# Kernel optimization log

Hardware: AMD Instinct MI355X
Metric: run time of the kernel (lower is better)

The kernel has to match this reference:

```python
import jax, jax.numpy as jnp
import numpy as np

DIM = 128; HEADS = 8; WS = 8; SHIFT = 4; B = 8; H = 256; W = 256; T = 1


def _rel_index(ws):
    # faithful port of create_relative_position_index
    coords = np.arange(ws)
    yy, xx = np.meshgrid(coords, coords, indexing='ij')
    cf = np.stack([yy.reshape(-1), xx.reshape(-1)])          # (2, ws*ws)
    rel = cf[:, :, None] - cf[:, None, :]                     # (2, N, N)
    rel[0] += ws - 1
    rel[1] += ws - 1
    return rel[0] * (2 * ws - 1) + rel[1]                     # (N, N) int


def _row_mask(ws, shift):
    jj, ii = np.meshgrid(np.arange(ws), np.arange(ws), indexing='ij')
    return ((jj >= ws - shift) | (ii >= ws - shift)).reshape(-1)  # (N,) bool


def layernorm(x, g, b, eps=1e-5):
    mu = x.mean(-1, keepdims=True)
    var = ((x - mu) ** 2).mean(-1, keepdims=True)
    return (x - mu) * jax.lax.rsqrt(var + eps) * g + b


def setup_inputs() -> dict:
    key = jax.random.key(0)
    ks = jax.random.split(key, 16)
    s = 0.02
    d = DIM
    inp = {
        'x': jax.random.normal(ks[0], (B, T, H, W, d), jnp.float32),
        'wq': jax.random.normal(ks[1], (d, d), jnp.float32) * s,
        'bq': jnp.zeros((d,), jnp.float32),
        'wk': jax.random.normal(ks[2], (d, d), jnp.float32) * s,
        'bk': jnp.zeros((d,), jnp.float32),
        'wv': jax.random.normal(ks[3], (d, d), jnp.float32) * s,
        'bv': jnp.zeros((d,), jnp.float32),
        'wp': jax.random.normal(ks[4], (d, d), jnp.float32) * s,
        'bp': jnp.zeros((d,), jnp.float32),
        'rpb': jax.random.normal(ks[5], (2 * WS - 1, 2 * WS - 1, HEADS), jnp.float32) * s,
        'ln1_g': jnp.ones((d,), jnp.float32),
        'ln1_b': jnp.zeros((d,), jnp.float32),
        'ln2_g': jnp.ones((d,), jnp.float32),
        'ln2_b': jnp.zeros((d,), jnp.float32),
        'w1': jax.random.normal(ks[6], (d, 4 * d), jnp.float32) * s,
        'b1': jnp.zeros((4 * d,), jnp.float32),
        'w2': jax.random.normal(ks[7], (4 * d, d), jnp.float32) * s,
        'b2': jnp.zeros((d,), jnp.float32),
        'gate': jax.random.normal(ks[8], (1, H, W, 1), jnp.float32) * s,
    }
    return inp


def reference(x, wq, bq, wk, bk, wv, bv, wp, bp, rpb, ln1_g, ln1_b, ln2_g, ln2_b, w1, b1, w2, b2, gate):
    Bx, Tx, Hx, Wx, C = x.shape
    skip = x[:, 0]                                             # (B,H,W,C)
    xn = layernorm(x, ln1_g, ln1_b)[:, 0]                      # (B,H,W,C)
    xs = jnp.roll(xn, (-SHIFT, -SHIFT), axis=(1, 2))
    nh, nw, N = Hx // WS, Wx // WS, WS * WS
    # window partition -> (B*nh*nw, N, C)
    xw = xs.reshape(Bx, nh, WS, nw, WS, C).transpose(0, 1, 3, 2, 4, 5).reshape(-1, N, C)
    hd = C // HEADS
    scale = hd ** -0.5
    q = (xw @ wq + bq).reshape(-1, N, HEADS, hd)
    k = (xw @ wk + bk).reshape(-1, N, HEADS, hd)
    v = (xw @ wv + bv).reshape(-1, N, HEADS, hd)
    attn = jnp.einsum('bnhc,bmhc->bnhm', q, k) * scale         # (Bw,N,H,N)
    # relative position bias gather; .view(B,N,heads,N) over (N*N,heads) flat layout
    idx = jnp.asarray(_rel_index(WS).reshape(-1))
    bias = rpb.reshape(-1, HEADS)[idx].reshape(N, HEADS, N)
    attn = attn + bias[None]
    # shift mask: full query rows set to -1e9 (per original patch_mask)
    rmask = jnp.asarray(_row_mask(WS, SHIFT))
    attn = jnp.where(rmask[None, :, None, None], jnp.float32(-1e9), attn)
    attn = jax.nn.softmax(attn, axis=-1)
    out = jnp.einsum('bnhm,bmhc->bnhc', attn, v).reshape(-1, N, C) @ wp + bp
    # window reverse
    xr = out.reshape(Bx, nh, nw, WS, WS, C).transpose(0, 1, 3, 2, 4, 5).reshape(Bx, Hx, Wx, C)
    xa = xs + xr
    xa = jnp.roll(xa, (SHIFT, SHIFT), axis=(1, 2))
    # gated skip
    x2 = xa + jax.nn.sigmoid(gate) * skip
    # MLP (dropout = identity in eval)
    h = jax.nn.gelu(layernorm(x2, ln2_g, ln2_b) @ w1 + b1, approximate=False)
    y = x2 + (h @ w2 + b2)
    return y.reshape(Bx, Tx, Hx, Wx, C)
```

## Files before the change

### kernel.cpp

```cpp
#include <hip/hip_runtime.h>
#include <hip/hip_bf16.h>
#include <math.h>

#define TPB 256

typedef __attribute__((ext_vector_type(8))) __bf16 bf16x8;
typedef __attribute__((ext_vector_type(4))) float f32x4;

static __device__ __forceinline__ bf16x8 lds_frag(const char* base, int row, int byteOff, int rowBytes) {
    return *reinterpret_cast<const bf16x8*>(base + row * rowBytes + (byteOff ^ ((row & 7) << 4)));
}
static __device__ __forceinline__ void lds_wr_bf16(char* base, int row, int col, int rowBytes, float v) {
    *reinterpret_cast<__bf16*>(base + row * rowBytes + ((col << 1) ^ ((row & 7) << 4))) = (__bf16)v;
}

__global__ void convert_w(const float* __restrict__ wq, const float* __restrict__ wk,
                          const float* __restrict__ wv, const float* __restrict__ wp,
                          const float* __restrict__ w1, const float* __restrict__ w2,
                          const float* __restrict__ rpb, const float* __restrict__ bq,
                          __bf16* __restrict__ ws)
{
    int g = blockIdx.x * 256 + threadIdx.x;
    if (g < 65536) {
        int which = g >> 14, idx = g & 16383, n = idx >> 7, k = idx & 127;
        const float* W = (which == 0) ? wq : (which == 1) ? wk : (which == 2) ? wv : wp;
        float v = W[k * 128 + n];
        if (which == 0) v *= 0.25f;
        ws[g] = (__bf16)v;
    } else if (g < 131072) {
        int idx = g - 65536, n = idx >> 7, k = idx & 127;
        ws[g] = (__bf16)w1[k * 512 + n];
    } else if (g < 196608) {
        int idx = g - 131072, n = idx >> 9, k = idx & 511;
        ws[g] = (__bf16)w2[k * 128 + n];
    } else if (g < 204800) {
        float* wsf = (float*)(ws + 196608);
        int g2 = g - 196608;
        int hc = g2 >> 8, h = hc >> 2, ct = hc & 3;
        int lane = (g2 >> 2) & 63, kg = lane >> 4, ar = lane & 15, r = g2 & 3;
        int dy = kg - h + 7;
        int dx = r - (ct * 2 + (ar >> 3)) + 7;
        wsf[g2] = rpb[(dy * 15 + dx) * 8 + (ar & 7)];
    } else if (g < 204928) {
        float* wsf = (float*)(ws + 196608);
        wsf[8192 + (g - 204800)] = bq[g - 204800] * 0.25f;
    }
}

#define O_K     0
#define O_VT    16384
#define O_XN    32768
#define O_H     16384
#define O_ATTN  49152
#define O_PROJ  57344
#define O_Q     66320
#define O_P     70416
#define O_MU    78608
#define O_RS    78864
#define O_GATE  79120
#define O_BASE  79376
#define SMEM_SZ 79632

__global__ __launch_bounds__(TPB, 2) void swin_fused_kernel(
    const float* __restrict__ x,
    const __bf16* __restrict__ wqT,
    const __bf16* __restrict__ wkT, const float* __restrict__ bk,
    const __bf16* __restrict__ wvT, const float* __restrict__ bv,
    const __bf16* __restrict__ wpT, const float* __restrict__ bp,
    const float* __restrict__ bias_pre, const float* __restrict__ bqs,
    const float* __restrict__ ln1g, const float* __restrict__ ln1b,
    const float* __restrict__ ln2g, const float* __restrict__ ln2b,
    const __bf16* __restrict__ w1T, const float* __restrict__ b1,
    const __bf16* __restrict__ w2T, const float* __restrict__ b2,
    const float* __restrict__ gate,
    float* __restrict__ out)
{
    __shared__ __align__(16) char smem[SMEM_SZ];
    char* s_k    = smem + O_K;
    char* s_vT   = smem + O_VT;
    char* s_xn   = smem + O_XN;
    char* s_h    = smem + O_H;
    char* s_attn = smem + O_ATTN;
    float* s_proj = (float*)(smem + O_PROJ);
    char* s_q    = smem + O_Q;
    float* s_out  = (float*)(smem);
    float* s_mu   = (float*)(smem + O_MU);
    float* s_rs   = (float*)(smem + O_RS);
    float* s_gate = (float*)(smem + O_GATE);
    int*   s_base = (int*)(smem + O_BASE);

    const int tid = threadIdx.x;
    const int blk = blockIdx.x;
    const int b  = blk >> 10;
    const int wh = (blk >> 5) & 31;
    const int ww = blk & 31;

    const int row = tid >> 2;
    const int l4  = tid & 3;
    float vals[32];

    {
        const int si = wh * 8 + (row >> 3), sj = ww * 8 + (row & 7);
        const int oi = (si + 4) & 255, oj = (sj + 4) & 255;
        const int base = ((b * 256 + oi) * 256 + oj) * 128;
        if (l4 == 0) { s_base[row] = base; s_gate[row] = gate[oi * 256 + oj]; }
        const float* xp = x + base + l4 * 32;
        float sum = 0.f, sq = 0.f;
#pragma unroll
        for (int i = 0; i < 8; ++i) {
            const float4 v4 = reinterpret_cast<const float4*>(xp)[i];
            vals[4*i+0] = v4.x; vals[4*i+1] = v4.y; vals[4*i+2] = v4.z; vals[4*i+3] = v4.w;
            sum += v4.x + v4.y + v4.z + v4.w;
            sq  += v4.x*v4.x + v4.y*v4.y + v4.z*v4.z + v4.w*v4.w;
        }
        sum += __shfl_xor(sum, 1); sum += __shfl_xor(sum, 2);
        sq  += __shfl_xor(sq , 1); sq  += __shfl_xor(sq , 2);
        const float mu  = sum * (1.f / 128.f);
        const float var = sq * (1.f / 128.f) - mu * mu;
        const float rs  = rsqrtf(var + 1e-5f);
        if (l4 == 0) { s_mu[row] = mu; s_rs[row] = rs; }
#pragma unroll
        for (int j = 0; j < 4; ++j) {
            bf16x8 pk;
#pragma unroll
            for (int e = 0; e < 8; ++e) {
                const int d = l4 * 32 + j * 8 + e;
                pk[e] = (__bf16)((vals[j*8+e] - mu) * rs * ln1g[d] + ln1b[d]);
            }
            const int byteOff = (l4 * 64 + j * 16) ^ ((row & 7) << 4);
            *reinterpret_cast<bf16x8*>(s_xn + row * 256 + byteOff) = pk;
        }
    }
    __syncthreads();

    const int lane = tid & 63, w = tid >> 6;
    const int ar = lane & 15, kg = lane >> 4;

    float vm[2];

    {
        bf16x8 a[4][4];
#pragma unroll
        for (int rt = 0; rt < 4; ++rt)
#pragma unroll
            for (int kc = 0; kc < 4; ++kc)
                a[rt][kc] = lds_frag(s_xn, rt * 16 + ar, kc * 64 + (kg << 4), 256);
        const int nrow = ((ar >> 2) << 3) + (ar & 3);
        bf16x8 aq[4];
#pragma unroll
        for (int kc = 0; kc < 4; ++kc)
            aq[kc] = lds_frag(s_xn, nrow, kc * 64 + (kg << 4), 256);

#pragma unroll
        for (int ct2 = 0; ct2 < 2; ++ct2) {
            const int brow = (w + ct2 * 4) * 16 + ar;
            bf16x8 bf[4];
#pragma unroll
            for (int kc = 0; kc < 4; ++kc)
                bf[kc] = *reinterpret_cast<const bf16x8*>(wkT + brow * 128 + kc * 32 + (kg << 3));
            const float bb = bk[brow];
#pragma unroll
            for (int rt = 0; rt < 4; ++rt) {
                f32x4 c = {bb, bb, bb, bb};
#pragma unroll
                for (int kc = 0; kc < 4; ++kc)
                    c = __builtin_amdgcn_mfma_f32_16x16x32_bf16(a[rt][kc], bf[kc], c, 0, 0, 0);
#pragma unroll
                for (int r = 0; r < 4; ++r)
                    lds_wr_bf16(s_k, rt*16 + kg*4 + r, brow, 256, c[r]);
            }
        }
#pragma unroll
        for (int ct2 = 0; ct2 < 2; ++ct2) {
            const int brow = (w + ct2 * 4) * 16 + ar;
            bf16x8 bf[4];
#pragma unroll
            for (int kc = 0; kc < 4; ++kc)
                bf[kc] = *reinterpret_cast<const bf16x8*>(wvT + brow * 128 + kc * 32 + (kg << 3));
            const float bb = bv[brow];
            float vs = 0.f;
#pragma unroll
            for (int rt = 0; rt < 4; ++rt) {
                f32x4 c = {bb, bb, bb, bb};
#pragma unroll
                for (int kc = 0; kc < 4; ++kc)
                    c = __builtin_amdgcn_mfma_f32_16x16x32_bf16(a[rt][kc], bf[kc], c, 0, 0, 0);
#pragma unroll
                for (int r = 0; r < 4; ++r) {
                    lds_wr_bf16(s_vT, brow, rt*16 + kg*4 + r, 128, c[r]);
                    vs += c[r];
                }
            }
            vs += __shfl_xor(vs, 16); vs += __shfl_xor(vs, 32);
            vm[ct2] = vs * (1.f / 64.f);
        }
#pragma unroll
        for (int ct2 = 0; ct2 < 2; ++ct2) {
            const int brow = (w + ct2 * 4) * 16 + ar;
            bf16x8 bf[4];
#pragma unroll
            for (int kc = 0; kc < 4; ++kc)
                bf[kc] = *reinterpret_cast<const bf16x8*>(wqT + brow * 128 + kc * 32 + (kg << 3));
            const float bb = bqs[brow];
            f32x4 c = {bb, bb, bb, bb};
#pragma unroll
            for (int kc = 0; kc < 4; ++kc)
                c = __builtin_amdgcn_mfma_f32_16x16x32_bf16(aq[kc], bf[kc], c, 0, 0, 0);
#pragma unroll
            for (int r = 0; r < 4; ++r)
                lds_wr_bf16(s_q, kg*4 + r, brow, 256, c[r]);
        }
    }
    __syncthreads();

    if (kg == 0) {
#pragma unroll
        for (int ct2 = 0; ct2 < 2; ++ct2)
            lds_wr_bf16(s_attn, 16, (w + ct2 * 4) * 16 + ar, 256, vm[ct2]);
    }

    char* s_p = smem + O_P + (w << 11);
#pragma unroll
    for (int hi = 0; hi < 2; ++hi) {
        const int h = w + hi * 4;
        bf16x8 aQ = {};
        if (lane < 32) aQ = lds_frag(s_q, ar, h * 32 + (kg << 4), 256);
        f32x4 sc[4];
#pragma unroll
        for (int ct = 0; ct < 4; ++ct) {
            bf16x8 bK = {};
            if (lane < 32) bK = lds_frag(s_k, ct * 16 + ar, h * 32 + (kg << 4), 256);
            const f32x4 cin = *reinterpret_cast<const f32x4*>(bias_pre + ((h * 4 + ct) << 8) + (lane << 2));
            sc[ct] = __builtin_amdgcn_mfma_f32_16x16x32_bf16(aQ, bK, cin, 0, 0, 0);
        }
        float s[4] = {0.f, 0.f, 0.f, 0.f};
#pragma unroll
        for (int ct = 0; ct < 4; ++ct)
#pragma unroll
            for (int r = 0; r < 4; ++r) {
                sc[ct][r] = __expf(sc[ct][r]);
                s[r] += sc[ct][r];
            }
#pragma unroll
        for (int r = 0; r < 4; ++r) {
            s[r] += __shfl_xor(s[r], 1); s[r] += __shfl_xor(s[r], 2);
            s[r] += __shfl_xor(s[r], 4); s[r] += __shfl_xor(s[r], 8);
            const float inv = 1.f / s[r];
#pragma unroll
            for (int ct = 0; ct < 4; ++ct)
                lds_wr_bf16(s_p, kg*4 + r, ct*16 + ar, 128, sc[ct][r] * inv);
        }
        f32x4 o = {0.f, 0.f, 0.f, 0.f};
#pragma unroll
        for (int kc = 0; kc < 2; ++kc) {
            bf16x8 ap = lds_frag(s_p, ar, kc * 64 + (kg << 4), 128);
            bf16x8 bV = lds_frag(s_vT, h * 16 + ar, kc * 64 + (kg << 4), 128);
            o = __builtin_amdgcn_mfma_f32_16x16x32_bf16(ap, bV, o, 0, 0, 0);
        }
#pragma unroll
        for (int r = 0; r < 4; ++r)
            lds_wr_bf16(s_attn, kg*4 + r, h*16 + ar, 256, o[r]);
    }
    __syncthreads();

    {
        bf16x8 a2[2][4];
#pragma unroll
        for (int rt = 0; rt < 2; ++rt)
#pragma unroll
            for (int kc = 0; kc < 4; ++kc)
                a2[rt][kc] = lds_frag(s_attn, rt * 16 + ar, kc * 64 + (kg << 4), 256);
#pragma unroll
        for (int ct2 = 0; ct2 < 2; ++ct2) {
            const int brow = (w + ct2 * 4) * 16 + ar;
            bf16x8 bf[4];
#pragma unroll
            for (int kc = 0; kc < 4; ++kc)
                bf[kc] = *reinterpret_cast<const bf16x8*>(wpT + brow * 128 + kc * 32 + (kg << 3));
            const float bb = bp[brow];
#pragma unroll
            for (int rt = 0; rt < 2; ++rt) {
                f32x4 c = {bb, bb, bb, bb};
#pragma unroll
                for (int kc = 0; kc < 4; ++kc)
                    c = __builtin_amdgcn_mfma_f32_16x16x32_bf16(a2[rt][kc], bf[kc], c, 0, 0, 0);
                if (rt == 0) {
#pragma unroll
                    for (int r = 0; r < 4; ++r)
                        s_proj[(kg*4 + r) * 132 + brow] = c[r];
                } else if (kg == 0) {
                    s_proj[16 * 132 + brow] = c[0];
                }
            }
        }
    }
    __syncthreads();

    {
        const float sg = 1.f / (1.f + __expf(-s_gate[row]));
        const float mu1 = s_mu[row], rs1 = s_rs[row];
        const bool masked = ((row >> 3) >= 4) || ((row & 7) >= 4);
        const int prow = masked ? 16 : ((row >> 3) * 4 + (row & 7));
        const float* pr = s_proj + prow * 132 + l4 * 32;
        const float* g1  = ln1g + l4 * 32;
        const float* b1v = ln1b + l4 * 32;
        float sum = 0.f, sq = 0.f;
#pragma unroll
        for (int i = 0; i < 8; ++i) {
            const float4 gg = reinterpret_cast<const float4*>(g1)[i];
            const float4 bb = reinterpret_cast<const float4*>(b1v)[i];
            const float g4[4] = {gg.x, gg.y, gg.z, gg.w};
            const float b4[4] = {bb.x, bb.y, bb.z, bb.w};
#pragma unroll
            for (int c = 0; c < 4; ++c) {
                const int idx = 4*i + c;
                const float xv = vals[idx];
                const float xnv = (xv - mu1) * rs1 * g4[c] + b4[c];
                const float x2 = xnv + pr[idx] + sg * xv;
                vals[idx] = x2;
                sum += x2; sq += x2 * x2;
            }
        }
        sum += __shfl_xor(sum, 1); sum += __shfl_xor(sum, 2);
        sq  += __shfl_xor(sq , 1); sq  += __shfl_xor(sq , 2);
        const float mu  = sum * (1.f / 128.f);
        const float var = sq * (1.f / 128.f) - mu * mu;
        const float rs  = rsqrtf(var + 1e-5f);
#pragma unroll
        for (int j = 0; j < 4; ++j) {
            bf16x8 pk;
#pragma unroll
            for (int e = 0; e < 8; ++e) {
                const int d = l4 * 32 + j * 8 + e;
                pk[e] = (__bf16)((vals[j*8+e] - mu) * rs * ln2g[d] + ln2b[d]);
            }
            const int byteOff = (l4 * 64 + j * 16) ^ ((row & 7) << 4);
            *reinterpret_cast<bf16x8*>(s_k + row * 256 + byteOff) = pk;
        }
    }
    __syncthreads();

    bf16x8 a[4][4];
#pragma unroll
    for (int rt = 0; rt < 4; ++rt)
#pragma unroll
        for (int kc = 0; kc < 4; ++kc)
            a[rt][kc] = lds_frag(s_k, rt * 16 + ar, kc * 64 + (kg << 4), 256);

    f32x4 acc2[2][4];
#pragma unroll
    for (int ct2 = 0; ct2 < 2; ++ct2) {
        const float bb = b2[(w + ct2 * 4) * 16 + ar];
#pragma unroll
        for (int rt = 0; rt < 4; ++rt) acc2[ct2][rt] = {bb, bb, bb, bb};
    }

#pragma unroll
    for (int hh = 0; hh < 2; ++hh) {
#pragma unroll
        for (int i = 0; i < 4; ++i) {
            const int ct = hh * 16 + w + 4 * i;
            const int brow = ct * 16 + ar;
            bf16x8 bfr[4];
#pragma unroll
            for (int kc = 0; kc < 4; ++kc)
                bfr[kc] = *reinterpret_cast<const bf16x8*>(w1T + brow * 128 + kc * 32 + (kg << 3));
            const float bb = b1[brow];
#pragma unroll
            for (int rt = 0; rt < 4; ++rt) {
                f32x4 c = {bb, bb, bb, bb};
#pragma unroll
                for (int kc = 0; kc < 4; ++kc)
                    c = __builtin_amdgcn_mfma_f32_16x16x32_bf16(a[rt][kc], bfr[kc], c, 0, 0, 0);
#pragma unroll
                for (int r = 0; r < 4; ++r) {
                    const float v = c[r];
                    const float t = 0.7978845608028654f * (v + 0.044715f * v * v * v);
                    const float th = 1.f - 2.f / (__expf(2.f * t) + 1.f);
                    lds_wr_bf16(s_h, rt * 16 + kg * 4 + r, brow - hh * 256, 512, 0.5f * v * (1.f + th));
                }
            }
        }
        __syncthreads();
#pragma unroll
        for (int kc = 0; kc < 8; ++kc) {
            bf16x8 ah[4];
#pragma unroll
            for (int rt = 0; rt < 4; ++rt)
                ah[rt] = lds_frag(s_h, rt * 16 + ar, kc * 64 + (kg << 4), 512);
#pragma unroll
            for (int ct2 = 0; ct2 < 2; ++ct2) {
                const int brow = (w + ct2 * 4) * 16 + ar;
                const bf16x8 bw = *reinterpret_cast<const bf16x8*>(w2T + brow * 512 + hh * 256 + kc * 32 + (kg << 3));
#pragma unroll
                for (int rt = 0; rt < 4; ++rt)
                    acc2[ct2][rt] = __builtin_amdgcn_mfma_f32_16x16x32_bf16(ah[rt], bw, acc2[ct2][rt], 0, 0, 0);
            }
        }
        __syncthreads();
    }

#pragma unroll
    for (int ct2 = 0; ct2 < 2; ++ct2)
#pragma unroll
        for (int rt = 0; rt < 4; ++rt)
#pragma unroll
            for (int r = 0; r < 4; ++r)
                s_out[(rt * 16 + kg * 4 + r) * 132 + (w + ct2 * 4) * 16 + ar] = acc2[ct2][rt][r];
    __syncthreads();
    {
        const int base = s_base[row];
        float* op = out + base + l4 * 32;
        const float* po = s_out + row * 132 + l4 * 32;
#pragma unroll
        for (int i = 0; i < 8; ++i) {
            float4 o;
            o.x = vals[4*i+0] + po[4*i+0];
            o.y = vals[4*i+1] + po[4*i+1];
            o.z = vals[4*i+2] + po[4*i+2];
            o.w = vals[4*i+3] + po[4*i+3];
            reinterpret_cast<float4*>(op)[i] = o;
        }
    }
}

extern "C" void kernel_launch(void* const* d_in, const int* in_sizes, int n_in,
                              void* d_out, int out_size, void* d_ws, size_t ws_size,
                              hipStream_t stream) {
    (void)in_sizes; (void)n_in; (void)ws_size; (void)out_size;
    const float* x    = (const float*)d_in[0];
    const float* wq   = (const float*)d_in[1];
    const float* bq   = (const float*)d_in[2];
    const float* wk   = (const float*)d_in[3];
    const float* bk   = (const float*)d_in[4];
    const float* wv   = (const float*)d_in[5];
    const float* bv   = (const float*)d_in[6];
    const float* wp   = (const float*)d_in[7];
    const float* bp   = (const float*)d_in[8];
    const float* rpb  = (const float*)d_in[9];
    const float* ln1g = (const float*)d_in[10];
    const float* ln1b = (const float*)d_in[11];
    const float* ln2g = (const float*)d_in[12];
    const float* ln2b = (const float*)d_in[13];
    const float* w1   = (const float*)d_in[14];
    const float* b1   = (const float*)d_in[15];
    const float* w2   = (const float*)d_in[16];
    const float* b2   = (const float*)d_in[17];
    const float* gate = (const float*)d_in[18];
    float* out = (float*)d_out;

    __bf16* ws = (__bf16*)d_ws;
    const __bf16* wqT = ws;
    const __bf16* wkT = ws + 16384;
    const __bf16* wvT = ws + 32768;
    const __bf16* wpT = ws + 49152;
    const __bf16* w1T = ws + 65536;
    const __bf16* w2T = ws + 131072;
    const float* wsf  = (const float*)(ws + 196608);
    const float* bias_pre = wsf;
    const float* bqs      = wsf + 8192;

    convert_w<<<801, 256, 0, stream>>>(wq, wk, wv, wp, w1, w2, rpb, bq, ws);
    swin_fused_kernel<<<8192, TPB, 0, stream>>>(x, wqT, wkT, bk, wvT, bv, wpT, bp,
                                                bias_pre, bqs, ln1g, ln1b, ln2g, ln2b,
                                                w1T, b1, w2T, b2, gate, out);
}
```

Before: 701.1 us.

## Swap MFMA operands for packed LDS writes and shrink shared memory for 3 blocks/CU

Several GEMMs now pass the weight tile as the A operand and the activation as B. Each lane then holds four consecutive output columns and can write them to LDS as one packed bf16x4 store instead of four scalar bf16 stores. The shared-memory layout is overlapped more tightly, cutting it from about 79.6KB to about 50.7KB, and launch bounds are raised to 3 blocks per CU. The masked-row output is now computed as the V-mean times Wp in a scalar loop, and the relative-bias precompute layout is permuted to match. The changes add an extra __syncthreads and register pressure under the tighter occupancy bound, which risks spills.

```diff
diff --git a/kernel.cpp b/kernel.cpp
--- a/kernel.cpp
+++ b/kernel.cpp
@@ -5,13 +5,16 @@
 #define TPB 256
 
 typedef __attribute__((ext_vector_type(8))) __bf16 bf16x8;
+typedef __attribute__((ext_vector_type(4))) __bf16 bf16x4;
 typedef __attribute__((ext_vector_type(4))) float f32x4;
 
 static __device__ __forceinline__ bf16x8 lds_frag(const char* base, int row, int byteOff, int rowBytes) {
     return *reinterpret_cast<const bf16x8*>(base + row * rowBytes + (byteOff ^ ((row & 7) << 4)));
 }
-static __device__ __forceinline__ void lds_wr_bf16(char* base, int row, int col, int rowBytes, float v) {
-    *reinterpret_cast<__bf16*>(base + row * rowBytes + ((col << 1) ^ ((row & 7) << 4))) = (__bf16)v;
+static __device__ __forceinline__ void lds_wr4(char* base, int row, int col0, int rowBytes, f32x4 v) {
+    bf16x4 p;
+    p[0] = (__bf16)v[0]; p[1] = (__bf16)v[1]; p[2] = (__bf16)v[2]; p[3] = (__bf16)v[3];
+    *reinterpret_cast<bf16x4*>(base + row * rowBytes + ((col0 << 1) ^ ((row & 7) << 4))) = p;
 }
 
 __global__ void convert_w(const float* __restrict__ wq, const float* __restrict__ wk,
@@ -38,30 +41,26 @@
         int g2 = g - 196608;
         int hc = g2 >> 8, h = hc >> 2, ct = hc & 3;
         int lane = (g2 >> 2) & 63, kg = lane >> 4, ar = lane & 15, r = g2 & 3;
-        int dy = kg - h + 7;
-        int dx = r - (ct * 2 + (ar >> 3)) + 7;
-        wsf[g2] = rpb[(dy * 15 + dx) * 8 + (ar & 7)];
+        int dy = (ar >> 2) - h + 7;
+        int dx = (ar & 3) - (ct * 2 + (kg >> 1)) + 7;
+        int hsrc = ((kg & 1) << 2) | r;
+        wsf[g2] = rpb[(dy * 15 + dx) * 8 + hsrc];
     } else if (g < 204928) {
         float* wsf = (float*)(ws + 196608);
         wsf[8192 + (g - 204800)] = bq[g - 204800] * 0.25f;
     }
 }
 
-#define O_K     0
-#define O_VT    16384
-#define O_XN    32768
-#define O_H     16384
-#define O_ATTN  49152
-#define O_PROJ  57344
-#define O_Q     66320
-#define O_P     70416
-#define O_MU    78608
-#define O_RS    78864
-#define O_GATE  79120
-#define O_BASE  79376
-#define SMEM_SZ 79632
-
-__global__ __launch_bounds__(TPB, 2) void swin_fused_kernel(
+#define O_P     4096
+#define O_ATTN  12288
+#define O_MU    49152
+#define O_RS    49408
+#define O_GATE  49664
+#define O_BASE  49920
+#define O_VMEAN 50176
+#define SMEM_SZ 50688
+
+__global__ __launch_bounds__(TPB, 3) void swin_fused_kernel(
     const float* __restrict__ x,
     const __bf16* __restrict__ wqT,
     const __bf16* __restrict__ wkT, const float* __restrict__ bk,
@@ -76,18 +75,20 @@
     float* __restrict__ out)
 {
     __shared__ __align__(16) char smem[SMEM_SZ];
-    char* s_k    = smem + O_K;
-    char* s_vT   = smem + O_VT;
-    char* s_xn   = smem + O_XN;
-    char* s_h    = smem + O_H;
+    char* s_xn   = smem;
+    char* s_q    = smem;
+    char* s_k    = smem + 16384;
+    char* s_vT   = smem + 32768;
+    char* s_xn2  = smem + 32768;
     char* s_attn = smem + O_ATTN;
-    float* s_proj = (float*)(smem + O_PROJ);
-    char* s_q    = smem + O_Q;
+    char* s_h    = smem;
+    float* s_proj = (float*)(smem);
     float* s_out  = (float*)(smem);
     float* s_mu   = (float*)(smem + O_MU);
     float* s_rs   = (float*)(smem + O_RS);
     float* s_gate = (float*)(smem + O_GATE);
     int*   s_base = (int*)(smem + O_BASE);
+    float* s_vmean = (float*)(smem + O_VMEAN);
 
     const int tid = threadIdx.x;
     const int blk = blockIdx.x;
@@ -136,46 +137,42 @@
     const int lane = tid & 63, w = tid >> 6;
     const int ar = lane & 15, kg = lane >> 4;
 
-    float vm[2];
-
-    {
-        bf16x8 a[4][4];
-#pragma unroll
-        for (int rt = 0; rt < 4; ++rt)
-#pragma unroll
-            for (int kc = 0; kc < 4; ++kc)
-                a[rt][kc] = lds_frag(s_xn, rt * 16 + ar, kc * 64 + (kg << 4), 256);
+    bf16x8 a[4][4];
+    bf16x8 aq[4];
+    {
+#pragma unroll
+        for (int nt = 0; nt < 4; ++nt)
+#pragma unroll
+            for (int kc = 0; kc < 4; ++kc)
+                a[nt][kc] = lds_frag(s_xn, nt * 16 + ar, kc * 64 + (kg << 4), 256);
         const int nrow = ((ar >> 2) << 3) + (ar & 3);
-        bf16x8 aq[4];
 #pragma unroll
         for (int kc = 0; kc < 4; ++kc)
             aq[kc] = lds_frag(s_xn, nrow, kc * 64 + (kg << 4), 256);
 
+#pragma unroll
+        for (int ct2 = 0; ct2 < 2; ++ct2) {
+            const int m0t = (w + ct2 * 4) * 16;
+            bf16x8 af[4];
+#pragma unroll
+            for (int kc = 0; kc < 4; ++kc)
+                af[kc] = *reinterpret_cast<const bf16x8*>(wkT + (m0t + ar) * 128 + kc * 32 + (kg << 3));
+            const float4 bb4 = *reinterpret_cast<const float4*>(bk + m0t + kg * 4);
+#pragma unroll
+            for (int nt = 0; nt < 4; ++nt) {
+                f32x4 c = {bb4.x, bb4.y, bb4.z, bb4.w};
+#pragma unroll
+                for (int kc = 0; kc < 4; ++kc)
+                    c = __builtin_amdgcn_mfma_f32_16x16x32_bf16(af[kc], a[nt][kc], c, 0, 0, 0);
+                lds_wr4(s_k, nt * 16 + ar, m0t + kg * 4, 256, c);
+            }
+        }
 #pragma unroll
         for (int ct2 = 0; ct2 < 2; ++ct2) {
             const int brow = (w + ct2 * 4) * 16 + ar;
             bf16x8 bf[4];
 #pragma unroll
             for (int kc = 0; kc < 4; ++kc)
-                bf[kc] = *reinterpret_cast<const bf16x8*>(wkT + brow * 128 + kc * 32 + (kg << 3));
-            const float bb = bk[brow];
-#pragma unroll
-            for (int rt = 0; rt < 4; ++rt) {
-                f32x4 c = {bb, bb, bb, bb};
-#pragma unroll
-                for (int kc = 0; kc < 4; ++kc)
-                    c = __builtin_amdgcn_mfma_f32_16x16x32_bf16(a[rt][kc], bf[kc], c, 0, 0, 0);
-#pragma unroll
-                for (int r = 0; r < 4; ++r)
-                    lds_wr_bf16(s_k, rt*16 + kg*4 + r, brow, 256, c[r]);
-            }
-        }
-#pragma unroll
-        for (int ct2 = 0; ct2 < 2; ++ct2) {
-            const int brow = (w + ct2 * 4) * 16 + ar;
-            bf16x8 bf[4];
-#pragma unroll
-            for (int kc = 0; kc < 4; ++kc)
                 bf[kc] = *reinterpret_cast<const bf16x8*>(wvT + brow * 128 + kc * 32 + (kg << 3));
             const float bb = bv[brow];
             float vs = 0.f;
@@ -185,39 +182,32 @@
 #pragma unroll
                 for (int kc = 0; kc < 4; ++kc)
                     c = __builtin_amdgcn_mfma_f32_16x16x32_bf16(a[rt][kc], bf[kc], c, 0, 0, 0);
-#pragma unroll
-                for (int r = 0; r < 4; ++r) {
-                    lds_wr_bf16(s_vT, brow, rt*16 + kg*4 + r, 128, c[r]);
-                    vs += c[r];
-                }
+                lds_wr4(s_vT, brow, rt * 16 + kg * 4, 128, c);
+                vs += c[0] + c[1] + c[2] + c[3];
             }
             vs += __shfl_xor(vs, 16); vs += __shfl_xor(vs, 32);
-            vm[ct2] = vs * (1.f / 64.f);
-        }
+            if (kg == 0) s_vmean[brow] = vs * (1.f / 64.f);
+        }
+    }
+    __syncthreads();
+
+    {
 #pragma unroll
         for (int ct2 = 0; ct2 < 2; ++ct2) {
-            const int brow = (w + ct2 * 4) * 16 + ar;
-            bf16x8 bf[4];
-#pragma unroll
-            for (int kc = 0; kc < 4; ++kc)
-                bf[kc] = *reinterpret_cast<const bf16x8*>(wqT + brow * 128 + kc * 32 + (kg << 3));
-            const float bb = bqs[brow];
-            f32x4 c = {bb, bb, bb, bb};
-#pragma unroll
-            for (int kc = 0; kc < 4; ++kc)
-                c = __builtin_amdgcn_mfma_f32_16x16x32_bf16(aq[kc], bf[kc], c, 0, 0, 0);
-#pragma unroll
-            for (int r = 0; r < 4; ++r)
-                lds_wr_bf16(s_q, kg*4 + r, brow, 256, c[r]);
-        }
-    }
-    __syncthreads();
-
-    if (kg == 0) {
-#pragma unroll
-        for (int ct2 = 0; ct2 < 2; ++ct2)
-            lds_wr_bf16(s_attn, 16, (w + ct2 * 4) * 16 + ar, 256, vm[ct2]);
-    }
+            const int m0t = (w + ct2 * 4) * 16;
+            bf16x8 af[4];
+#pragma unroll
+            for (int kc = 0; kc < 4; ++kc)
+                af[kc] = *reinterpret_cast<const bf16x8*>(wqT + (m0t + ar) * 128 + kc * 32 + (kg << 3));
+            const float4 bb4 = *reinterpret_cast<const float4*>(bqs + m0t + kg * 4);
+            f32x4 c = {bb4.x, bb4.y, bb4.z, bb4.w};
+#pragma unroll
+            for (int kc = 0; kc < 4; ++kc)
+                c = __builtin_amdgcn_mfma_f32_16x16x32_bf16(af[kc], aq[kc], c, 0, 0, 0);
+            lds_wr4(s_q, ar, m0t + kg * 4, 256, c);
+        }
+    }
+    __syncthreads();
 
     char* s_p = smem + O_P + (w << 11);
 #pragma unroll
@@ -231,45 +221,39 @@
             bf16x8 bK = {};
             if (lane < 32) bK = lds_frag(s_k, ct * 16 + ar, h * 32 + (kg << 4), 256);
             const f32x4 cin = *reinterpret_cast<const f32x4*>(bias_pre + ((h * 4 + ct) << 8) + (lane << 2));
-            sc[ct] = __builtin_amdgcn_mfma_f32_16x16x32_bf16(aQ, bK, cin, 0, 0, 0);
-        }
-        float s[4] = {0.f, 0.f, 0.f, 0.f};
+            sc[ct] = __builtin_amdgcn_mfma_f32_16x16x32_bf16(bK, aQ, cin, 0, 0, 0);
+        }
+        float sm = 0.f;
 #pragma unroll
         for (int ct = 0; ct < 4; ++ct)
 #pragma unroll
             for (int r = 0; r < 4; ++r) {
                 sc[ct][r] = __expf(sc[ct][r]);
-                s[r] += sc[ct][r];
-            }
-#pragma unroll
-        for (int r = 0; r < 4; ++r) {
-            s[r] += __shfl_xor(s[r], 1); s[r] += __shfl_xor(s[r], 2);
-            s[r] += __shfl_xor(s[r], 4); s[r] += __shfl_xor(s[r], 8);
-            const float inv = 1.f / s[r];
-#pragma unroll
-            for (int ct = 0; ct < 4; ++ct)
-                lds_wr_bf16(s_p, kg*4 + r, ct*16 + ar, 128, sc[ct][r] * inv);
+                sm += sc[ct][r];
+            }
+        sm += __shfl_xor(sm, 16); sm += __shfl_xor(sm, 32);
+        const float inv = 1.f / sm;
+#pragma unroll
+        for (int ct = 0; ct < 4; ++ct) {
+            f32x4 p4 = {sc[ct][0] * inv, sc[ct][1] * inv, sc[ct][2] * inv, sc[ct][3] * inv};
+            lds_wr4(s_p, ar, ct * 16 + kg * 4, 128, p4);
         }
         f32x4 o = {0.f, 0.f, 0.f, 0.f};
 #pragma unroll
         for (int kc = 0; kc < 2; ++kc) {
-            bf16x8 ap = lds_frag(s_p, ar, kc * 64 + (kg << 4), 128);
+            bf16x8 ap = lds_frag(s_p,  ar, kc * 64 + (kg << 4), 128);
             bf16x8 bV = lds_frag(s_vT, h * 16 + ar, kc * 64 + (kg << 4), 128);
-            o = __builtin_amdgcn_mfma_f32_16x16x32_bf16(ap, bV, o, 0, 0, 0);
-        }
-#pragma unroll
-        for (int r = 0; r < 4; ++r)
-            lds_wr_bf16(s_attn, kg*4 + r, h*16 + ar, 256, o[r]);
-    }
-    __syncthreads();
-
-    {
-        bf16x8 a2[2][4];
-#pragma unroll
-        for (int rt = 0; rt < 2; ++rt)
-#pragma unroll
-            for (int kc = 0; kc < 4; ++kc)
-                a2[rt][kc] = lds_frag(s_attn, rt * 16 + ar, kc * 64 + (kg << 4), 256);
+            o = __builtin_amdgcn_mfma_f32_16x16x32_bf16(bV, ap, o, 0, 0, 0);
+        }
+        lds_wr4(s_attn, ar, h * 16 + kg * 4, 256, o);
+    }
+    __syncthreads();
+
+    {
+        bf16x8 a2[4];
+#pragma unroll
+        for (int kc = 0; kc < 4; ++kc)
+            a2[kc] = lds_frag(s_attn, ar, kc * 64 + (kg << 4), 256);
 #pragma unroll
         for (int ct2 = 0; ct2 < 2; ++ct2) {
             const int brow = (w + ct2 * 4) * 16 + ar;
@@ -278,20 +262,25 @@
             for (int kc = 0; kc < 4; ++kc)
                 bf[kc] = *reinterpret_cast<const bf16x8*>(wpT + brow * 128 + kc * 32 + (kg << 3));
             const float bb = bp[brow];
-#pragma unroll
-            for (int rt = 0; rt < 2; ++rt) {
-                f32x4 c = {bb, bb, bb, bb};
-#pragma unroll
-                for (int kc = 0; kc < 4; ++kc)
-                    c = __builtin_amdgcn_mfma_f32_16x16x32_bf16(a2[rt][kc], bf[kc], c, 0, 0, 0);
-                if (rt == 0) {
-#pragma unroll
-                    for (int r = 0; r < 4; ++r)
-                        s_proj[(kg*4 + r) * 132 + brow] = c[r];
-                } else if (kg == 0) {
-                    s_proj[16 * 132 + brow] = c[0];
-                }
-            }
+            f32x4 c = {bb, bb, bb, bb};
+#pragma unroll
+            for (int kc = 0; kc < 4; ++kc)
+                c = __builtin_amdgcn_mfma_f32_16x16x32_bf16(a2[kc], bf[kc], c, 0, 0, 0);
+#pragma unroll
+            for (int r = 0; r < 4; ++r)
+                s_proj[(kg * 4 + r) * 132 + brow] = c[r];
+        }
+        if (tid < 128) {
+            const int col = tid;
+            float acc = bp[col];
+#pragma unroll
+            for (int j = 0; j < 16; ++j) {
+                const bf16x8 w8 = *reinterpret_cast<const bf16x8*>(wpT + col * 128 + j * 8);
+#pragma unroll
+                for (int e = 0; e < 8; ++e)
+                    acc += s_vmean[j * 8 + e] * (float)w8[e];
+            }
+            s_proj[16 * 132 + col] = acc;
         }
     }
     __syncthreads();
@@ -326,6 +315,7 @@
         const float mu  = sum * (1.f / 128.f);
         const float var = sq * (1.f / 128.f) - mu * mu;
         const float rs  = rsqrtf(var + 1e-5f);
+        __syncthreads();
 #pragma unroll
         for (int j = 0; j < 4; ++j) {
             bf16x8 pk;
@@ -335,17 +325,17 @@
                 pk[e] = (__bf16)((vals[j*8+e] - mu) * rs * ln2g[d] + ln2b[d]);
             }
             const int byteOff = (l4 * 64 + j * 16) ^ ((row & 7) << 4);
-            *reinterpret_cast<bf16x8*>(s_k + row * 256 + byteOff) = pk;
-        }
-    }
-    __syncthreads();
-
-    bf16x8 a[4][4];
-#pragma unroll
-    for (int rt = 0; rt < 4; ++rt)
+            *reinterpret_cast<bf16x8*>(s_xn2 + row * 256 + byteOff) = pk;
+        }
+    }
+    __syncthreads();
+
+    bf16x8 bx[4][4];
+#pragma unroll
+    for (int nt = 0; nt < 4; ++nt)
 #pragma unroll
         for (int kc = 0; kc < 4; ++kc)
-            a[rt][kc] = lds_frag(s_k, rt * 16 + ar, kc * 64 + (kg << 4), 256);
+            bx[nt][kc] = lds_frag(s_xn2, nt * 16 + ar, kc * 64 + (kg << 4), 256);
 
     f32x4 acc2[2][4];
 #pragma unroll
@@ -359,26 +349,28 @@
     for (int hh = 0; hh < 2; ++hh) {
 #pragma unroll
         for (int i = 0; i < 4; ++i) {
-            const int ct = hh * 16 + w + 4 * i;
-            const int brow = ct * 16 + ar;
-            bf16x8 bfr[4];
-#pragma unroll
-            for (int kc = 0; kc < 4; ++kc)
-                bfr[kc] = *reinterpret_cast<const bf16x8*>(w1T + brow * 128 + kc * 32 + (kg << 3));
-            const float bb = b1[brow];
-#pragma unroll
-            for (int rt = 0; rt < 4; ++rt) {
-                f32x4 c = {bb, bb, bb, bb};
+            const int hcol0 = (w + 4 * i) * 16;
+            const int m0g = hh * 256 + hcol0;
+            bf16x8 af[4];
+#pragma unroll
+            for (int kc = 0; kc < 4; ++kc)
+                af[kc] = *reinterpret_cast<const bf16x8*>(w1T + (m0g + ar) * 128 + kc * 32 + (kg << 3));
+            const float4 bb4 = *reinterpret_cast<const float4*>(b1 + m0g + kg * 4);
+#pragma unroll
+            for (int nt = 0; nt < 4; ++nt) {
+                f32x4 c = {bb4.x, bb4.y, bb4.z, bb4.w};
 #pragma unroll
                 for (int kc = 0; kc < 4; ++kc)
-                    c = __builtin_amdgcn_mfma_f32_16x16x32_bf16(a[rt][kc], bfr[kc], c, 0, 0, 0);
+                    c = __builtin_amdgcn_mfma_f32_16x16x32_bf16(af[kc], bx[nt][kc], c, 0, 0, 0);
+                f32x4 g4;
 #pragma unroll
                 for (int r = 0; r < 4; ++r) {
                     const float v = c[r];
                     const float t = 0.7978845608028654f * (v + 0.044715f * v * v * v);
                     const float th = 1.f - 2.f / (__expf(2.f * t) + 1.f);
-                    lds_wr_bf16(s_h, rt * 16 + kg * 4 + r, brow - hh * 256, 512, 0.5f * v * (1.f + th));
+                    g4[r] = 0.5f * v * (1.f + th);
                 }
+                lds_wr4(s_h, nt * 16 + ar, hcol0 + kg * 4, 512, g4);
             }
         }
         __syncthreads();
```

Result: slower. 745.8 us (+6.4%).
